# Optimization experiments

Hardware: AMD Instinct MI355X
Metric: run time of the kernel (lower is better)

## Reference

```python
import jax, jax.numpy as jnp
import numpy as np

B, Q, P = 8, 300, 5
RS, QS, CS, NC = 256, 768, 768, 396
HW = [64, 32, 16, 8]
POOL = [32, 16, 8, 4]
THR = 0.2


def _ln(x, g, b, eps=1e-5):
    m = x.mean(-1, keepdims=True)
    v = ((x - m) ** 2).mean(-1, keepdims=True)
    return (x - m) / jnp.sqrt(v + eps) * g + b


def _avgpool(x, oh, ow):
    # exact adaptive avg pool (output divides input)
    b, c, h, w = x.shape
    return x.reshape(b, c, oh, h // oh, ow, w // ow).mean((3, 5))


def setup_inputs() -> dict:
    key = jax.random.key(0)
    ks = jax.random.split(key, 40)
    inp = {}
    inp['pred_logits'] = jax.random.normal(ks[0], (B, Q, P), dtype=jnp.float32)
    inp['pred_boxes'] = jax.random.uniform(ks[1], (B, Q, 4), dtype=jnp.float32)
    inp['hs'] = jax.random.normal(ks[2], (B, Q, RS), dtype=jnp.float32)
    for s in range(4):
        inp[f'feat{s}'] = jax.random.normal(ks[3 + s], (B, 256, HW[s], HW[s]), dtype=jnp.float32)
        inp[f'pos{s}'] = jax.random.normal(ks[7 + s], (B, 256, HW[s], HW[s]), dtype=jnp.float32)
        inp[f'mask{s}'] = jax.random.bernoulli(ks[11 + s], 0.15, (B, HW[s], HW[s]))
        inp[f'convW{s}'] = jax.random.normal(ks[15 + s], (CS, 256), dtype=jnp.float32) * 0.02
        inp[f'convb{s}'] = jnp.zeros((CS,), jnp.float32)
        inp[f'lng{s}'] = jnp.ones((CS,), jnp.float32)
        inp[f'lnb{s}'] = jnp.zeros((CS,), jnp.float32)
    inp['learnable_query'] = jax.random.normal(ks[19], (P + 1, QS), dtype=jnp.float32)
    inp['Wq'] = jax.random.normal(ks[20], (RS, QS), dtype=jnp.float32) * 0.02
    inp['bq'] = jnp.zeros((QS,), jnp.float32)
    inp['qng'] = jnp.ones((QS,), jnp.float32)
    inp['qnb'] = jnp.zeros((QS,), jnp.float32)
    inp['W1'] = jax.random.normal(ks[21], (QS, QS), dtype=jnp.float32) * 0.02
    inp['b1'] = jnp.zeros((QS,), jnp.float32)
    inp['W2'] = jax.random.normal(ks[22], (QS, NC), dtype=jnp.float32) * 0.02
    inp['b2'] = jnp.zeros((NC,), jnp.float32)
    return inp


def _forward(pred_logits, pred_boxes, hs,
             feats, poss, masks, convWs, convbs, lngs, lnbs,
             learnable_query, Wq, bq, qng, qnb, W1, b1, W2, b2):
    del pred_boxes  # selected in the original but never used
    b = hs.shape[0]
    prob = jax.nn.sigmoid(pred_logits)                       # (B,Q,P)
    # per-prompt membership: logit_i > thr (implies max > thr)
    m = (prob > THR).astype(hs.dtype)                        # (B,Q,P)
    cnt = m.sum(1)                                           # (B,P)
    ssum = jnp.einsum('bqp,bqd->bpd', m, hs)                 # segment-sum over queries
    pooled = jnp.where(cnt[..., None] > 0,
                       ssum / jnp.maximum(cnt, 1.0)[..., None], 0.0)  # (B,P,RS)
    proj = pooled @ Wq + bq                                  # (B,P,QS)
    any_sel = jnp.any(prob.max(-1) > THR, axis=1)            # (B,)
    # if no query passed the global gate, prompt_hs is zeros WITHOUT projection
    prompt_hs = jnp.where(any_sel[:, None, None], proj, 0.0)
    prompt_query = learnable_query[1:] + prompt_hs           # (B,P,QS)
    cls_query = jnp.broadcast_to(learnable_query[0][None, None, :], (b, 1, QS))
    query_tokens = jnp.concatenate([cls_query, prompt_query], axis=1)
    query_tokens = _ln(query_tokens, qng, qnb)               # (B,P+1,QS)

    tokens = []
    for s in range(4):
        mask_f = masks[s][:, None, :, :].astype(feats[s].dtype)   # (B,1,H,W)
        x = (feats[s] + poss[s]) * (1.0 - mask_f)                 # masked_fill
        ctx = jnp.einsum('bchw,oc->bohw', x, convWs[s]) + convbs[s][None, :, None, None]
        p = _avgpool(ctx, POOL[s], POOL[s])
        mp = jnp.clip(_avgpool(1.0 - mask_f, POOL[s], POOL[s]), 1e-6, None)
        p = p / mp
        t = p.reshape(b, CS, -1).transpose(0, 2, 1)               # (B,T_s,CS)
        tokens.append(_ln(t, lngs[s], lnbs[s]))
    ctx_all = jnp.concatenate(tokens, axis=1)                     # (B,1360,CS)

    # encoder stand-in: fuse context into query tokens additively
    last = query_tokens + ctx_all.mean(1)[:, None, :]
    cls_logit = last[:, 0]
    prompt_logit = last[:, 1:].mean(1)
    h = jax.nn.relu((cls_logit + prompt_logit) @ W1 + b1)
    return h @ W2 + b2                                            # (B,NC)


def reference(pred_logits, pred_boxes, hs,
              feat0, pos0, mask0, convW0, convb0, lng0, lnb0,
              feat1, pos1, mask1, convW1, convb1, lng1, lnb1,
              feat2, pos2, mask2, convW2, convb2, lng2, lnb2,
              feat3, pos3, mask3, convW3, convb3, lng3, lnb3,
              learnable_query, Wq, bq, qng, qnb, W1, b1, W2, b2):
    return _forward(pred_logits, pred_boxes, hs,
                    [feat0, feat1, feat2, feat3],
                    [pos0, pos1, pos2, pos3],
                    [mask0, mask1, mask2, mask3],
                    [convW0, convW1, convW2, convW3],
                    [convb0, convb1, convb2, convb3],
                    [lng0, lng1, lng2, lng3],
                    [lnb0, lnb1, lnb2, lnb3],
                    learnable_query, Wq, bq, qng, qnb, W1, b1, W2, b2)
```

## Files before the change

### kernel.cpp

```cpp
#include <hip/hip_runtime.h>
#include <hip/hip_bf16.h>

#define Bn 8
#define Qn 300
#define Pn 5
#define RSn 256
#define QSn 768
#define NCn 396
#define MTOT 10880
#define THRL -1.3862943611198906f

typedef __attribute__((ext_vector_type(8))) short short8;
typedef __attribute__((ext_vector_type(4))) float float4v;

__device__ inline float wred(float v){
  #pragma unroll
  for (int off = 32; off; off >>= 1) v += __shfl_xor(v, off);
  return v;
}

__device__ __forceinline__ unsigned short f2bf(float f){
  union { float f; unsigned int u; } c; c.f = f;
  return (unsigned short)((c.u + 0x7FFF + ((c.u >> 16) & 1)) >> 16);
}

__device__ __forceinline__ void gld_lds16(const short* g, short* l){
  __builtin_amdgcn_global_load_lds(
      (const __attribute__((address_space(1))) void*)g,
      (__attribute__((address_space(3))) void*)l, 16, 0, 0);
}

__global__ __launch_bounds__(256, 4) void k_front(
    const float* cw0, const float* cw1, const float* cw2, const float* cw3,
    short* Wswz, const int* __restrict__ mk0, int* det,
    const float* __restrict__ pl, const float* __restrict__ hs,
    float* pooled, int* flags, float* ctxsum, float* outz){
  int bx = blockIdx.x;
  int t = threadIdx.x;
  if (bx < 768){
    int s = bx / 192;
    int linear = (bx % 192)*256 + t;
    int q = linear & 63, n = linear >> 6;
    const float* src = (s==0)?cw0:(s==1)?cw1:(s==2)?cw2:cw3;
    float4 f = *(const float4*)(src + (size_t)n*256 + q*4);
    int kc = q >> 3, lk = (q >> 1) & 3, e0 = (q & 1)*4;
    short* dst = Wswz + ((size_t)(s*8 + kc))*24576 + lk*6144 + n*8 + e0;
    short4 sv;
    sv.x = (short)f2bf(f.x); sv.y = (short)f2bf(f.y);
    sv.z = (short)f2bf(f.z); sv.w = (short)f2bf(f.w);
    *(short4*)dst = sv;
    return;
  }
  if (bx == 768){
    __shared__ int r0[4], r1[4];
    const int* mm = mk0 + t*32;
    int d0 = 0, d1 = 0;
    #pragma unroll 8
    for (int i = 0; i < 32; ++i){
      int v = mm[i];
      d0 |= (v != 0 && v != 1);
      d1 |= (v != 0 && v != 0x3F800000);
    }
    unsigned long long bal0 = __ballot(d0), bal1 = __ballot(d1);
    int wid = t >> 6;
    if ((t & 63) == 0){ r0[wid] = (bal0 != 0ull); r1[wid] = (bal1 != 0ull); }
    __syncthreads();
    if (t == 0){
      det[0] = r0[0] | r0[1] | r0[2] | r0[3];
      det[1] = r1[0] | r1[1] | r1[2] | r1[3];
    }
    return;
  }
  if (bx >= 821){
    int idx = ((bx - 821)*256 + t)*4;
    if (idx < Bn*NCn) *(float4*)(outz + idx) = (float4){0.f,0.f,0.f,0.f};
    return;
  }
  if (bx >= 809){
    int idx = ((bx - 809)*256 + t)*4;
    *(float4*)(ctxsum + idx) = (float4){0.f,0.f,0.f,0.f};
    return;
  }
  __shared__ float msk[Qn];
  int bb = (bx - 769) / Pn, p = (bx - 769) % Pn;
  for (int q = t; q < Qn; q += 256)
    msk[q] = (pl[(bb*Qn + q)*Pn + p] > THRL) ? 1.f : 0.f;
  __syncthreads();
  const float* hb = hs + (size_t)bb*Qn*RSn + t;
  float s0 = 0.f, s1 = 0.f, s2 = 0.f, s3 = 0.f, cnt = 0.f;
  for (int q = 0; q < Qn; q += 4){
    float m0v = msk[q], m1 = msk[q+1], m2 = msk[q+2], m3 = msk[q+3];
    cnt += m0v + m1 + m2 + m3;
    s0 = fmaf(m0v, hb[(size_t)(q  )*RSn], s0);
    s1 = fmaf(m1,  hb[(size_t)(q+1)*RSn], s1);
    s2 = fmaf(m2,  hb[(size_t)(q+2)*RSn], s2);
    s3 = fmaf(m3,  hb[(size_t)(q+3)*RSn], s3);
  }
  float ssum = (s0 + s1) + (s2 + s3);
  pooled[(bb*Pn + p)*RSn + t] = (cnt > 0.f) ? ssum / cnt : 0.f;
  if (t == 0) flags[bb*Pn + p] = (cnt > 0.f) ? 1 : 0;
}

__global__ __launch_bounds__(256, 2) void k_pgemm(
    const float* fe0, const float* po0, const void* ma0,
    const float* fe1, const float* po1, const void* ma1,
    const float* fe2, const float* po2, const void* ma2,
    const float* fe3, const float* po3, const void* ma3,
    const int* __restrict__ det, const short* __restrict__ Wswz,
    const float* cb0, const float* cb1, const float* cb2, const float* cb3,
    const float* lg0, const float* lb0, const float* lg1, const float* lb1,
    const float* lg2, const float* lb2, const float* lg3, const float* lb3,
    float* __restrict__ ctxsum,
    const float* __restrict__ lq, const float* __restrict__ Wq,
    const float* __restrict__ bq, const float* __restrict__ qng,
    const float* __restrict__ qnb, const float* __restrict__ pooled,
    const int* __restrict__ flags, float* qt){
  __shared__ short Bsh[24576];
  __shared__ short As[32*264];
  __shared__ float wls[32][4];
  __shared__ float scls[32], imls[32];
  __shared__ float lsum[4][32], lsq[4][32];
  __shared__ float pq[256];
  __shared__ float s1s[4], s2s[4];
  int blk = blockIdx.x;
  int t = threadIdx.x;

  if (blk >= 340){
    int qbx = blk - 340;
    int b = qbx / 6, j = qbx % 6;
    float v0 = lq[j*QSn + t], v1 = lq[j*QSn + t + 256], v2 = lq[j*QSn + t + 512];
    int any = flags[b*Pn] | flags[b*Pn+1] | flags[b*Pn+2] | flags[b*Pn+3] | flags[b*Pn+4];
    if (j > 0 && any){
      pq[t] = pooled[(b*Pn + (j-1))*RSn + t];
      __syncthreads();
      float a0 = 0.f, a1 = 0.f, a2 = 0.f;
      #pragma unroll 8
      for (int c = 0; c < RSn; ++c){
        float pv = pq[c];
        a0 = fmaf(pv, Wq[c*QSn + t      ], a0);
        a1 = fmaf(pv, Wq[c*QSn + t + 256], a1);
        a2 = fmaf(pv, Wq[c*QSn + t + 512], a2);
      }
      v0 += a0 + bq[t]; v1 += a1 + bq[t+256]; v2 += a2 + bq[t+512];
    }
    float sm = v0 + v1 + v2, sq = v0*v0 + v1*v1 + v2*v2;
    sm = wred(sm); sq = wred(sq);
    int wid = t >> 6, lane = t & 63;
    if (lane == 0){ s1s[wid] = sm; s2s[wid] = sq; }
    __syncthreads();
    float S  = s1s[0] + s1s[1] + s1s[2] + s1s[3];
    float SQ = s2s[0] + s2s[1] + s2s[2] + s2s[3];
    float mu = S * (1.f/QSn), var = SQ * (1.f/QSn) - mu*mu;
    float rs = rsqrtf(var + 1e-5f);
    float* o = qt + (b*6 + j)*QSn;
    o[t      ] = (v0 - mu)*rs*qng[t      ] + qnb[t      ];
    o[t + 256] = (v1 - mu)*rs*qng[t + 256] + qnb[t + 256];
    o[t + 512] = (v2 - mu)*rs*qng[t + 512] + qnb[t + 512];
    return;
  }

  int m0 = blk * 32;
  int s, H, OWlog, b0, b1;
  const float *F, *Pp; const void* M;
  const float *CB, *LG, *LB;
  if (m0 < 8192){ s=0; F=fe0; Pp=po0; M=ma0; H=64; OWlog=5; b0=m0>>10; b1=b0;
                  CB=cb0; LG=lg0; LB=lb0; }
  else if (m0 < 10240){ s=1; F=fe1; Pp=po1; M=ma1; H=32; OWlog=4; b0=(m0-8192)>>8; b1=b0;
                  CB=cb1; LG=lg1; LB=lb1; }
  else if (m0 < 10752){ s=2; F=fe2; Pp=po2; M=ma2; H=16; OWlog=3; b0=(m0-10240)>>6; b1=b0;
                  CB=cb2; LG=lg2; LB=lb2; }
  else { s=3; F=fe3; Pp=po3; M=ma3; H=8; OWlog=2; b0=(m0-10752)>>4; b1=b0+1;
                  CB=cb3; LG=lg3; LB=lb3; }
  int HH = H*H;
  int OWm = (H >> 1) - 1;
  int mode = (det[0] == 0) ? 0 : ((det[1] == 0) ? 2 : 1);

  int slot = t & 31;
  int gm = m0 + slot;
  int bb, ltl;
  if (s == 0){ bb = gm >> 10; ltl = gm & 1023; }
  else if (s == 1){ bb = (gm - 8192) >> 8; ltl = gm & 255; }
  else if (s == 2){ bb = (gm - 10240) >> 6; ltl = gm & 63; }
  else { bb = (gm - 10752) >> 4; ltl = gm & 15; }
  int ph = ltl >> OWlog, pw = ltl & OWm;
  int i00 = ph*2*H + pw*2;
  int mbase = bb*HH;

  if (t < 32){
    float w0, w1, w2, w3;
    if (mode == 0){
      const int* Mi = (const int*)M + mbase + i00;
      int2 ma = *(const int2*)(Mi);
      int2 mb = *(const int2*)(Mi + H);
      w0 = ma.x?0.f:1.f; w1 = ma.y?0.f:1.f; w2 = mb.x?0.f:1.f; w3 = mb.y?0.f:1.f;
    } else if (mode == 1){
      const unsigned char* Mb = (const unsigned char*)M + mbase + i00;
      w0 = Mb[0]?0.f:1.f; w1 = Mb[1]?0.f:1.f; w2 = Mb[H]?0.f:1.f; w3 = Mb[H+1]?0.f:1.f;
    } else {
      const float* Mf = (const float*)M + mbase + i00;
      float2 ma = *(const float2*)(Mf);
      float2 mb = *(const float2*)(Mf + H);
      w0 = 1.f-ma.x; w1 = 1.f-ma.y; w2 = 1.f-mb.x; w3 = 1.f-mb.y;
    }
    float msum = w0 + w1 + w2 + w3;
    float im = 1.f / fmaxf(msum*0.25f, 1e-6f);
    wls[t][0] = w0; wls[t][1] = w1; wls[t][2] = w2; wls[t][3] = w3;
    scls[t] = 0.25f*im; imls[t] = im;
  }
  __syncthreads();

  {
    float w0 = wls[slot][0], w1 = wls[slot][1], w2 = wls[slot][2], w3 = wls[slot][3];
    float sc = scls[slot];
    int chb = (t >> 5) * 2;
    size_t base = (size_t)(bb*256 + chb)*HH + i00;
    const float* Fp = F + base;
    const float* Pq = Pp + base;
    const int stride = 16*HH;
    #pragma unroll 2
    for (int r = 0; r < 16; ++r){
      float2 fa0 = *(const float2*)(Fp);
      float2 fb0 = *(const float2*)(Fp + H);
      float2 pa0 = *(const float2*)(Pq);
      float2 pb0 = *(const float2*)(Pq + H);
      float2 fa1 = *(const float2*)(Fp + HH);
      float2 fb1 = *(const float2*)(Fp + HH + H);
      float2 pa1 = *(const float2*)(Pq + HH);
      float2 pb1 = *(const float2*)(Pq + HH + H);
      float x0 = (fa0.x+pa0.x)*w0 + (fa0.y+pa0.y)*w1 + (fb0.x+pb0.x)*w2 + (fb0.y+pb0.y)*w3;
      float x1 = (fa1.x+pa1.x)*w0 + (fa1.y+pa1.y)*w1 + (fb1.x+pb1.x)*w2 + (fb1.y+pb1.y)*w3;
      *(unsigned int*)(&As[slot*264 + chb + r*16]) =
          (unsigned int)f2bf(x0*sc) | ((unsigned int)f2bf(x1*sc) << 16);
      Fp += stride; Pq += stride;
    }
  }
  __syncthreads();

  int wid = t >> 6, l = t & 63;
  int lm = l & 15, lk = l >> 4;
  int nfb = wid * 12;
  short8 aReg[2][8];
  #pragma unroll
  for (int mt = 0; mt < 2; ++mt)
    #pragma unroll
    for (int kc = 0; kc < 8; ++kc)
      aReg[mt][kc] = *(const short8*)(As + (mt*16 + lm)*264 + kc*32 + lk*8);

  float4v acc[2][12];
  #pragma unroll
  for (int mt = 0; mt < 2; ++mt)
    #pragma unroll
    for (int nf = 0; nf < 12; ++nf) acc[mt][nf] = (float4v){0.f,0.f,0.f,0.f};

  #pragma unroll
  for (int kc = 0; kc < 8; ++kc){
    const short* slice = Wswz + ((size_t)(s*8 + kc))*24576;
    #pragma unroll
    for (int j = 0; j < 12; ++j){
      int chunk = wid*12 + j;
      gld_lds16(slice + chunk*512 + l*8, Bsh + chunk*512);
    }
    __syncthreads();
    const short* bb2 = Bsh + lk*6144 + lm*8;
    #pragma unroll
    for (int nf = 0; nf < 12; ++nf){
      short8 bf = *(const short8*)(bb2 + (size_t)(nfb+nf)*128);
      acc[0][nf] = __builtin_amdgcn_mfma_f32_16x16x32_bf16(aReg[0][kc], bf, acc[0][nf], 0, 0, 0);
      acc[1][nf] = __builtin_amdgcn_mfma_f32_16x16x32_bf16(aReg[1][kc], bf, acc[1][nf], 0, 0, 0);
    }
    __syncthreads();
  }

  float im[2][4];
  #pragma unroll
  for (int mt = 0; mt < 2; ++mt)
    #pragma unroll
    for (int r = 0; r < 4; ++r) im[mt][r] = imls[mt*16 + lk*4 + r];

  float sum[2][4] = {{0,0,0,0},{0,0,0,0}}, sq[2][4] = {{0,0,0,0},{0,0,0,0}};
  #pragma unroll
  for (int nf = 0; nf < 12; ++nf){
    float cbv = CB[(nfb+nf)*16 + lm];
    #pragma unroll
    for (int mt = 0; mt < 2; ++mt)
      #pragma unroll
      for (int r = 0; r < 4; ++r){
        float p = acc[mt][nf][r] + cbv*im[mt][r];
        acc[mt][nf][r] = p;
        sum[mt][r] += p;
        sq[mt][r] = fmaf(p, p, sq[mt][r]);
      }
  }
  #pragma unroll
  for (int mt = 0; mt < 2; ++mt)
    #pragma unroll
    for (int r = 0; r < 4; ++r){
      #pragma unroll
      for (int off = 1; off < 16; off <<= 1){
        sum[mt][r] += __shfl_xor(sum[mt][r], off);
        sq[mt][r]  += __shfl_xor(sq[mt][r],  off);
      }
    }
  if (lm == 0){
    #pragma unroll
    for (int mt = 0; mt < 2; ++mt)
      #pragma unroll
      for (int r = 0; r < 4; ++r){
        lsum[wid][mt*16 + lk*4 + r] = sum[mt][r];
        lsq[wid][mt*16 + lk*4 + r]  = sq[mt][r];
      }
  }
  __syncthreads();
  float mu[2][4], rs[2][4];
  #pragma unroll
  for (int mt = 0; mt < 2; ++mt)
    #pragma unroll
    for (int r = 0; r < 4; ++r){
      int row = mt*16 + lk*4 + r;
      float S  = lsum[0][row] + lsum[1][row] + lsum[2][row] + lsum[3][row];
      float SQ = lsq[0][row]  + lsq[1][row]  + lsq[2][row]  + lsq[3][row];
      mu[mt][r] = S * (1.f/768.f);
      float var = SQ * (1.f/768.f) - mu[mt][r]*mu[mt][r];
      rs[mt][r] = rsqrtf(var + 1e-5f);
    }
  #pragma unroll
  for (int nf = 0; nf < 12; ++nf){
    int n = (nfb+nf)*16 + lm;
    float g = LG[n], bv = LB[n];
    float tv0 = 0.f, tv1 = 0.f;
    #pragma unroll
    for (int r = 0; r < 4; ++r){
      tv0 += (acc[0][nf][r] - mu[0][r]) * rs[0][r];
      tv1 += (acc[1][nf][r] - mu[1][r]) * rs[1][r];
    }
    tv0 = tv0*g + 4.f*bv;
    tv1 = tv1*g + 4.f*bv;
    tv0 += __shfl_xor(tv0, 16); tv0 += __shfl_xor(tv0, 32);
    tv1 += __shfl_xor(tv1, 16); tv1 += __shfl_xor(tv1, 32);
    if (lk == 0){
      atomicAdd(&ctxsum[b0*768 + n], tv0);
      atomicAdd(&ctxsum[b1*768 + n], tv1);
    }
  }
}

__global__ void k_hpre(const float* __restrict__ qt, const float* __restrict__ ctxsum,
                       const float* __restrict__ W1, const float* __restrict__ b1,
                       float* __restrict__ hpre){
  __shared__ float vsh[Bn][192];
  int nc = blockIdx.x % 24, kc = blockIdx.x / 24;
  int n0 = nc*32, c0 = kc*192;
  int t = threadIdx.x;
  for (int i = t; i < Bn*192; i += 256){
    int b = i / 192, cl = i - b*192;
    int c = c0 + cl;
    const float* q = qt + (size_t)b*6*768;
    float pm = q[768+c] + q[2*768+c] + q[3*768+c] + q[4*768+c] + q[5*768+c];
    vsh[b][cl] = q[c] + 0.2f*pm + ctxsum[b*768 + c]*(1.f/680.f);
  }
  __syncthreads();
  int ow = t & 31, bi = t >> 5;
  int o = n0 + ow;
  float acc = 0.f;
  const float* w = W1 + (size_t)c0*768 + o;
  #pragma unroll 4
  for (int cl = 0; cl < 192; ++cl)
    acc = fmaf(vsh[bi][cl], w[(size_t)cl*768], acc);
  if (kc == 0) acc += b1[o];
  atomicAdd(&hpre[bi*768 + o], acc);
}

__global__ void k_out(const float* __restrict__ hpre, const float* __restrict__ W2,
                      const float* __restrict__ b2, float* __restrict__ out){
  __shared__ float hsh[Bn][192];
  int nc = blockIdx.x % 13, kc = blockIdx.x / 13;
  int n0 = nc*32, c0 = kc*192;
  int t = threadIdx.x;
  for (int i = t; i < Bn*192; i += 256){
    int b = i / 192, cl = i - b*192;
    hsh[b][cl] = fmaxf(hpre[b*768 + c0 + cl], 0.f);
  }
  __syncthreads();
  int ow = t & 31, bi = t >> 5;
  int o = n0 + ow;
  if (o >= NCn) return;
  float acc = 0.f;
  const float* w = W2 + (size_t)c0*NCn + o;
  #pragma unroll 4
  for (int cl = 0; cl < 192; ++cl)
    acc = fmaf(hsh[bi][cl], w[(size_t)cl*NCn], acc);
  if (kc == 0) acc += b2[o];
  atomicAdd(&out[bi*NCn + o], acc);
}

extern "C" void kernel_launch(void* const* d_in, const int* in_sizes, int n_in,
                              void* d_out, int out_size, void* d_ws, size_t ws_size,
                              hipStream_t stream){
  const float* pl = (const float*)d_in[0];
  const float* hs = (const float*)d_in[2];
  const float* feat[4]; const float* pos[4]; const void* mask[4];
  const float* cw[4]; const float* cb[4]; const float* lg[4]; const float* lb[4];
  for (int s = 0; s < 4; ++s){
    int base = 3 + 7*s;
    feat[s] = (const float*)d_in[base];
    pos[s]  = (const float*)d_in[base+1];
    mask[s] = d_in[base+2];
    cw[s]   = (const float*)d_in[base+3];
    cb[s]   = (const float*)d_in[base+4];
    lg[s]   = (const float*)d_in[base+5];
    lb[s]   = (const float*)d_in[base+6];
  }
  const float* lq  = (const float*)d_in[31];
  const float* Wq  = (const float*)d_in[32];
  const float* bq  = (const float*)d_in[33];
  const float* qng = (const float*)d_in[34];
  const float* qnb = (const float*)d_in[35];
  const float* W1  = (const float*)d_in[36];
  const float* b1  = (const float*)d_in[37];
  const float* W2  = (const float*)d_in[38];
  const float* b2  = (const float*)d_in[39];
  float* out = (float*)d_out;

  short* Wswz   = (short*)d_ws;
  float* pooled = (float*)(Wswz + (size_t)4*8*4*768*8);
  float* qt     = pooled + 40*RSn;
  float* ctxsum = qt + Bn*6*QSn;
  float* hpre   = ctxsum + Bn*QSn;
  int*   det    = (int*)(hpre + Bn*QSn);
  int*   flags  = det + 4;

  k_front<<<825, 256, 0, stream>>>(cw[0], cw[1], cw[2], cw[3], Wswz,
                                   (const int*)mask[0], det, pl, hs, pooled, flags,
                                   ctxsum, out);
  k_pgemm<<<388, 256, 0, stream>>>(feat[0], pos[0], mask[0],
                                   feat[1], pos[1], mask[1],
                                   feat[2], pos[2], mask[2],
                                   feat[3], pos[3], mask[3],
                                   det, Wswz,
                                   cb[0], cb[1], cb[2], cb[3],
                                   lg[0], lb[0], lg[1], lb[1],
                                   lg[2], lb[2], lg[3], lb[3], ctxsum,
                                   lq, Wq, bq, qng, qnb, pooled, flags, qt);
  k_hpre<<<96, 256, 0, stream>>>(qt, ctxsum, W1, b1, hpre);
  k_out<<<52, 256, 0, stream>>>(hpre, W2, b2, out);
}
```

Baseline: 269.1 us.

## Halve pooled-GEMM row tile and read B fragments directly from global

The pooled projection GEMM now processes 16 rows per block instead of 32, doubling the grid to 680 GEMM blocks so more workgroups spread across the CUs, and raises the occupancy hint to 3 blocks per SIMD group. The 48KB LDS staging buffer for the swizzled weights and its per-k barriers are removed; each wave loads its B fragments straight from global memory (L2-cached) into MFMA operands. The trade-off is that every weight byte is now fetched from global/L2 by twice as many blocks with no LDS reuse, and there are twice as many atomic adds into the context sum.

```diff
diff --git a/kernel.cpp b/kernel.cpp
--- a/kernel.cpp
+++ b/kernel.cpp
@@ -22,12 +22,6 @@
 __device__ __forceinline__ unsigned short f2bf(float f){
   union { float f; unsigned int u; } c; c.f = f;
   return (unsigned short)((c.u + 0x7FFF + ((c.u >> 16) & 1)) >> 16);
-}
-
-__device__ __forceinline__ void gld_lds16(const short* g, short* l){
-  __builtin_amdgcn_global_load_lds(
-      (const __attribute__((address_space(1))) void*)g,
-      (__attribute__((address_space(3))) void*)l, 16, 0, 0);
 }
 
 __global__ __launch_bounds__(256, 4) void k_front(
@@ -101,7 +95,7 @@
   if (t == 0) flags[bb*Pn + p] = (cnt > 0.f) ? 1 : 0;
 }
 
-__global__ __launch_bounds__(256, 2) void k_pgemm(
+__global__ __launch_bounds__(256, 3) void k_pgemm(
     const float* fe0, const float* po0, const void* ma0,
     const float* fe1, const float* po1, const void* ma1,
     const float* fe2, const float* po2, const void* ma2,
@@ -115,18 +109,17 @@
     const float* __restrict__ bq, const float* __restrict__ qng,
     const float* __restrict__ qnb, const float* __restrict__ pooled,
     const int* __restrict__ flags, float* qt){
-  __shared__ short Bsh[24576];
-  __shared__ short As[32*264];
-  __shared__ float wls[32][4];
-  __shared__ float scls[32], imls[32];
-  __shared__ float lsum[4][32], lsq[4][32];
+  __shared__ short As[16*264];
+  __shared__ float wls[16][4];
+  __shared__ float scls[16], imls[16];
+  __shared__ float lsum[4][16], lsq[4][16];
   __shared__ float pq[256];
   __shared__ float s1s[4], s2s[4];
   int blk = blockIdx.x;
   int t = threadIdx.x;
 
-  if (blk >= 340){
-    int qbx = blk - 340;
+  if (blk >= 680){
+    int qbx = blk - 680;
     int b = qbx / 6, j = qbx % 6;
     float v0 = lq[j*QSn + t], v1 = lq[j*QSn + t + 256], v2 = lq[j*QSn + t + 512];
     int any = flags[b*Pn] | flags[b*Pn+1] | flags[b*Pn+2] | flags[b*Pn+3] | flags[b*Pn+4];
@@ -159,34 +152,35 @@
     return;
   }
 
-  int m0 = blk * 32;
-  int s, H, OWlog, b0, b1;
+  int m0 = blk * 16;
+  int s, H, OWlog, b0;
   const float *F, *Pp; const void* M;
   const float *CB, *LG, *LB;
-  if (m0 < 8192){ s=0; F=fe0; Pp=po0; M=ma0; H=64; OWlog=5; b0=m0>>10; b1=b0;
+  if (m0 < 8192){ s=0; F=fe0; Pp=po0; M=ma0; H=64; OWlog=5; b0=m0>>10;
                   CB=cb0; LG=lg0; LB=lb0; }
-  else if (m0 < 10240){ s=1; F=fe1; Pp=po1; M=ma1; H=32; OWlog=4; b0=(m0-8192)>>8; b1=b0;
+  else if (m0 < 10240){ s=1; F=fe1; Pp=po1; M=ma1; H=32; OWlog=4; b0=(m0-8192)>>8;
                   CB=cb1; LG=lg1; LB=lb1; }
-  else if (m0 < 10752){ s=2; F=fe2; Pp=po2; M=ma2; H=16; OWlog=3; b0=(m0-10240)>>6; b1=b0;
+  else if (m0 < 10752){ s=2; F=fe2; Pp=po2; M=ma2; H=16; OWlog=3; b0=(m0-10240)>>6;
                   CB=cb2; LG=lg2; LB=lb2; }
-  else { s=3; F=fe3; Pp=po3; M=ma3; H=8; OWlog=2; b0=(m0-10752)>>4; b1=b0+1;
+  else { s=3; F=fe3; Pp=po3; M=ma3; H=8; OWlog=2; b0=(m0-10752)>>4;
                   CB=cb3; LG=lg3; LB=lb3; }
   int HH = H*H;
   int OWm = (H >> 1) - 1;
   int mode = (det[0] == 0) ? 0 : ((det[1] == 0) ? 2 : 1);
 
-  int slot = t & 31;
+  int slot = t & 15;
   int gm = m0 + slot;
-  int bb, ltl;
-  if (s == 0){ bb = gm >> 10; ltl = gm & 1023; }
-  else if (s == 1){ bb = (gm - 8192) >> 8; ltl = gm & 255; }
-  else if (s == 2){ bb = (gm - 10240) >> 6; ltl = gm & 63; }
-  else { bb = (gm - 10752) >> 4; ltl = gm & 15; }
+  int bb = b0;
+  int ltl;
+  if (s == 0)      ltl = gm & 1023;
+  else if (s == 1) ltl = gm & 255;
+  else if (s == 2) ltl = gm & 63;
+  else             ltl = gm & 15;
   int ph = ltl >> OWlog, pw = ltl & OWm;
   int i00 = ph*2*H + pw*2;
   int mbase = bb*HH;
 
-  if (t < 32){
+  if (t < 16){
     float w0, w1, w2, w3;
     if (mode == 0){
       const int* Mi = (const int*)M + mbase + i00;
@@ -212,13 +206,13 @@
   {
     float w0 = wls[slot][0], w1 = wls[slot][1], w2 = wls[slot][2], w3 = wls[slot][3];
     float sc = scls[slot];
-    int chb = (t >> 5) * 2;
+    int chb = (t >> 4) * 2;
     size_t base = (size_t)(bb*256 + chb)*HH + i00;
     const float* Fp = F + base;
     const float* Pq = Pp + base;
-    const int stride = 16*HH;
+    const int stride = 32*HH;
     #pragma unroll 2
-    for (int r = 0; r < 16; ++r){
+    for (int r = 0; r < 8; ++r){
       float2 fa0 = *(const float2*)(Fp);
       float2 fb0 = *(const float2*)(Fp + H);
       float2 pa0 = *(const float2*)(Pq);
@@ -229,7 +223,7 @@
       float2 pb1 = *(const float2*)(Pq + HH + H);
       float x0 = (fa0.x+pa0.x)*w0 + (fa0.y+pa0.y)*w1 + (fb0.x+pb0.x)*w2 + (fb0.y+pb0.y)*w3;
       float x1 = (fa1.x+pa1.x)*w0 + (fa1.y+pa1.y)*w1 + (fb1.x+pb1.x)*w2 + (fb1.y+pb1.y)*w3;
-      *(unsigned int*)(&As[slot*264 + chb + r*16]) =
+      *(unsigned int*)(&As[slot*264 + chb + r*32]) =
           (unsigned int)f2bf(x0*sc) | ((unsigned int)f2bf(x1*sc) << 16);
       Fp += stride; Pq += stride;
     }
@@ -239,108 +233,80 @@
   int wid = t >> 6, l = t & 63;
   int lm = l & 15, lk = l >> 4;
   int nfb = wid * 12;
-  short8 aReg[2][8];
-  #pragma unroll
-  for (int mt = 0; mt < 2; ++mt)
-    #pragma unroll
-    for (int kc = 0; kc < 8; ++kc)
-      aReg[mt][kc] = *(const short8*)(As + (mt*16 + lm)*264 + kc*32 + lk*8);
-
-  float4v acc[2][12];
-  #pragma unroll
-  for (int mt = 0; mt < 2; ++mt)
-    #pragma unroll
-    for (int nf = 0; nf < 12; ++nf) acc[mt][nf] = (float4v){0.f,0.f,0.f,0.f};
-
+  short8 aReg[8];
+  #pragma unroll
+  for (int kc = 0; kc < 8; ++kc)
+    aReg[kc] = *(const short8*)(As + lm*264 + kc*32 + lk*8);
+
+  float4v acc[12];
+  #pragma unroll
+  for (int nf = 0; nf < 12; ++nf) acc[nf] = (float4v){0.f,0.f,0.f,0.f};
+
+  const short* Bb = Wswz + ((size_t)(s*8))*24576 + lk*6144 + nfb*128 + lm*8;
   #pragma unroll
   for (int kc = 0; kc < 8; ++kc){
-    const short* slice = Wswz + ((size_t)(s*8 + kc))*24576;
-    #pragma unroll
-    for (int j = 0; j < 12; ++j){
-      int chunk = wid*12 + j;
-      gld_lds16(slice + chunk*512 + l*8, Bsh + chunk*512);
-    }
-    __syncthreads();
-    const short* bb2 = Bsh + lk*6144 + lm*8;
+    const short* bp = Bb + kc*24576;
     #pragma unroll
     for (int nf = 0; nf < 12; ++nf){
-      short8 bf = *(const short8*)(bb2 + (size_t)(nfb+nf)*128);
-      acc[0][nf] = __builtin_amdgcn_mfma_f32_16x16x32_bf16(aReg[0][kc], bf, acc[0][nf], 0, 0, 0);
-      acc[1][nf] = __builtin_amdgcn_mfma_f32_16x16x32_bf16(aReg[1][kc], bf, acc[1][nf], 0, 0, 0);
-    }
-    __syncthreads();
-  }
-
-  float im[2][4];
-  #pragma unroll
-  for (int mt = 0; mt < 2; ++mt)
-    #pragma unroll
-    for (int r = 0; r < 4; ++r) im[mt][r] = imls[mt*16 + lk*4 + r];
-
-  float sum[2][4] = {{0,0,0,0},{0,0,0,0}}, sq[2][4] = {{0,0,0,0},{0,0,0,0}};
+      short8 bf = *(const short8*)(bp + nf*128);
+      acc[nf] = __builtin_amdgcn_mfma_f32_16x16x32_bf16(aReg[kc], bf, acc[nf], 0, 0, 0);
+    }
+  }
+
+  float im4[4];
+  #pragma unroll
+  for (int r = 0; r < 4; ++r) im4[r] = imls[lk*4 + r];
+
+  float sum[4] = {0,0,0,0}, sq[4] = {0,0,0,0};
   #pragma unroll
   for (int nf = 0; nf < 12; ++nf){
     float cbv = CB[(nfb+nf)*16 + lm];
     #pragma unroll
-    for (int mt = 0; mt < 2; ++mt)
-      #pragma unroll
-      for (int r = 0; r < 4; ++r){
-        float p = acc[mt][nf][r] + cbv*im[mt][r];
-        acc[mt][nf][r] = p;
-        sum[mt][r] += p;
-        sq[mt][r] = fmaf(p, p, sq[mt][r]);
-      }
-  }
-  #pragma unroll
-  for (int mt = 0; mt < 2; ++mt)
+    for (int r = 0; r < 4; ++r){
+      float p = acc[nf][r] + cbv*im4[r];
+      acc[nf][r] = p;
+      sum[r] += p;
+      sq[r] = fmaf(p, p, sq[r]);
+    }
+  }
+  #pragma unroll
+  for (int r = 0; r < 4; ++r){
+    #pragma unroll
+    for (int off = 1; off < 16; off <<= 1){
+      sum[r] += __shfl_xor(sum[r], off);
+      sq[r]  += __shfl_xor(sq[r],  off);
+    }
+  }
+  if (lm == 0){
     #pragma unroll
     for (int r = 0; r < 4; ++r){
-      #pragma unroll
-      for (int off = 1; off < 16; off <<= 1){
-        sum[mt][r] += __shfl_xor(sum[mt][r], off);
-        sq[mt][r]  += __shfl_xor(sq[mt][r],  off);
-      }
-    }
-  if (lm == 0){
-    #pragma unroll
-    for (int mt = 0; mt < 2; ++mt)
-      #pragma unroll
-      for (int r = 0; r < 4; ++r){
-        lsum[wid][mt*16 + lk*4 + r] = sum[mt][r];
-        lsq[wid][mt*16 + lk*4 + r]  = sq[mt][r];
-      }
-  }
-  __syncthreads();
-  float mu[2][4], rs[2][4];
-  #pragma unroll
-  for (int mt = 0; mt < 2; ++mt)
-    #pragma unroll
-    for (int r = 0; r < 4; ++r){
-      int row = mt*16 + lk*4 + r;
-      float S  = lsum[0][row] + lsum[1][row] + lsum[2][row] + lsum[3][row];
-      float SQ = lsq[0][row]  + lsq[1][row]  + lsq[2][row]  + lsq[3][row];
-      mu[mt][r] = S * (1.f/768.f);
-      float var = SQ * (1.f/768.f) - mu[mt][r]*mu[mt][r];
-      rs[mt][r] = rsqrtf(var + 1e-5f);
-    }
+      lsum[wid][lk*4 + r] = sum[r];
+      lsq[wid][lk*4 + r]  = sq[r];
+    }
+  }
+  __syncthreads();
+  float mu[4], rs[4];
+  #pragma unroll
+  for (int r = 0; r < 4; ++r){
+    int row = lk*4 + r;
+    float S  = lsum[0][row] + lsum[1][row] + lsum[2][row] + lsum[3][row];
+    float SQ = lsq[0][row]  + lsq[1][row]  + lsq[2][row]  + lsq[3][row];
+    mu[r] = S * (1.f/768.f);
+    float var = SQ * (1.f/768.f) - mu[r]*mu[r];
+    rs[r] = rsqrtf(var + 1e-5f);
+  }
   #pragma unroll
   for (int nf = 0; nf < 12; ++nf){
     int n = (nfb+nf)*16 + lm;
     float g = LG[n], bv = LB[n];
-    float tv0 = 0.f, tv1 = 0.f;
+    float tv = 0.f;
     #pragma unroll
-    for (int r = 0; r < 4; ++r){
-      tv0 += (acc[0][nf][r] - mu[0][r]) * rs[0][r];
-      tv1 += (acc[1][nf][r] - mu[1][r]) * rs[1][r];
-    }
-    tv0 = tv0*g + 4.f*bv;
-    tv1 = tv1*g + 4.f*bv;
-    tv0 += __shfl_xor(tv0, 16); tv0 += __shfl_xor(tv0, 32);
-    tv1 += __shfl_xor(tv1, 16); tv1 += __shfl_xor(tv1, 32);
-    if (lk == 0){
-      atomicAdd(&ctxsum[b0*768 + n], tv0);
-      atomicAdd(&ctxsum[b1*768 + n], tv1);
-    }
+    for (int r = 0; r < 4; ++r)
+      tv += (acc[nf][r] - mu[r]) * rs[r];
+    tv = tv*g + 4.f*bv;
+    tv += __shfl_xor(tv, 16); tv += __shfl_xor(tv, 32);
+    if (lk == 0)
+      atomicAdd(&ctxsum[b0*768 + n], tv);
   }
 }
 
@@ -432,7 +398,7 @@
   k_front<<<825, 256, 0, stream>>>(cw[0], cw[1], cw[2], cw[3], Wswz,
                                    (const int*)mask[0], det, pl, hs, pooled, flags,
                                    ctxsum, out);
-  k_pgemm<<<388, 256, 0, stream>>>(feat[0], pos[0], mask[0],
+  k_pgemm<<<728, 256, 0, stream>>>(feat[0], pos[0], mask[0],
                                    feat[1], pos[1], mask[1],
                                    feat[2], pos[2], mask[2],
                                    feat[3], pos[3], mask[3],
```

New measurement: 269.5 us. Within noise of the previous version (+0.2%).
